# Kernel optimization log

Measured on AMD Instinct MI355X. Metric: run time of the kernel, lower is better.

## Reference

```python
import jax, jax.numpy as jnp
import numpy as np
import math

BN, NA, NE = 8192, 15, 16
DO, DA, DE = 96, 88, 80
H, NH = 512, 8
A_MOVE = 6


def _mha(q_in, kv, mask, Wq, Wk, Wv, Wo, n_heads):
    # q_in: [B,H] single query; kv: [B,L,H]; mask: [B,L] bool (True = valid)
    B, Hd = q_in.shape
    Hh = Hd // n_heads
    q = (q_in @ Wq).reshape(B, n_heads, 1, Hh)
    k = (kv @ Wk).reshape(B, -1, n_heads, Hh).transpose(0, 2, 1, 3)  # [B,nh,L,Hh]
    v = (kv @ Wv).reshape(B, -1, n_heads, Hh).transpose(0, 2, 1, 3)
    scores = jnp.einsum('bhqd,bhkd->bhqk', q, k) / math.sqrt(Hh)
    scores = jnp.where(mask[:, None, None, :], scores, -1e9)
    attn = jax.nn.softmax(scores, axis=-1)
    out = jnp.einsum('bhqk,bhkd->bhqd', attn, v).reshape(B, Hd)
    return out @ Wo


def _gru_cell(x, h, W_ih, W_hh, b_ih, b_hh):
    # torch GRU cell math. x: [B,3H], h: [B,H]
    gi = x @ W_ih.T + b_ih  # [B,3H]
    gh = h @ W_hh.T + b_hh  # [B,3H]
    i_r, i_z, i_n = jnp.split(gi, 3, axis=-1)
    h_r, h_z, h_n = jnp.split(gh, 3, axis=-1)
    r = jax.nn.sigmoid(i_r + h_r)
    z = jax.nn.sigmoid(i_z + h_z)
    n = jnp.tanh(i_n + r * h_n)
    return (1.0 - z) * n + z * h


def setup_inputs() -> dict:
    key = jax.random.key(0)
    ks = jax.random.split(key, 24)
    s = 0.02
    inp = {
        'own': jax.random.normal(ks[0], (BN, 1, DO), jnp.float32),
        'ally': jax.random.normal(ks[1], (BN, NA, DA), jnp.float32),
        'enemy': jax.random.normal(ks[2], (BN, NE, DE), jnp.float32),
        'prev_h': jax.random.normal(ks[3], (BN, H), jnp.float32),
        'W_own': jax.random.normal(ks[4], (DO, H), jnp.float32) * s,
        'b_own': jnp.zeros((H,), jnp.float32),
        'W_ally': jax.random.normal(ks[5], (DA, H), jnp.float32) * s,
        'b_ally': jnp.zeros((H,), jnp.float32),
        'W_enemy': jax.random.normal(ks[6], (DE, H), jnp.float32) * s,
        'b_enemy': jnp.zeros((H,), jnp.float32),
        'Wq_a': jax.random.normal(ks[7], (H, H), jnp.float32) * s,
        'Wk_a': jax.random.normal(ks[8], (H, H), jnp.float32) * s,
        'Wv_a': jax.random.normal(ks[9], (H, H), jnp.float32) * s,
        'Wo_a': jax.random.normal(ks[10], (H, H), jnp.float32) * s,
        'Wq_e': jax.random.normal(ks[11], (H, H), jnp.float32) * s,
        'Wk_e': jax.random.normal(ks[12], (H, H), jnp.float32) * s,
        'Wv_e': jax.random.normal(ks[13], (H, H), jnp.float32) * s,
        'Wo_e': jax.random.normal(ks[14], (H, H), jnp.float32) * s,
        'W_ih': jax.random.normal(ks[15], (3 * H, 3 * H), jnp.float32) * s,
        'W_hh': jax.random.normal(ks[16], (3 * H, H), jnp.float32) * s,
        'b_ih': jnp.zeros((3 * H,), jnp.float32),
        'b_hh': jnp.zeros((3 * H,), jnp.float32),
        'W_q': jax.random.normal(ks[17], (H, A_MOVE + NE), jnp.float32) * s,
        'b_q': jnp.zeros((A_MOVE + NE,), jnp.float32),
    }
    return inp


def reference(own, ally, enemy, prev_h,
              W_own, b_own, W_ally, b_ally, W_enemy, b_enemy,
              Wq_a, Wk_a, Wv_a, Wo_a, Wq_e, Wk_e, Wv_e, Wo_e,
              W_ih, W_hh, b_ih, b_hh, W_q, b_q):
    # masks: entity valid iff not all-zero feature row
    ally_mask = ~jnp.all(ally == 0, axis=-1)    # [B,NA]
    enemy_mask = ~jnp.all(enemy == 0, axis=-1)  # [B,NE]

    e_own = (own @ W_own + b_own)[:, 0, :]      # [B,H]
    A = ally @ W_ally + b_ally                   # [B,NA,H]
    E = enemy @ W_enemy + b_enemy                # [B,NE,H]

    zA = _mha(e_own, A, ally_mask, Wq_a, Wk_a, Wv_a, Wo_a, NH)
    zE = _mha(e_own, E, enemy_mask, Wq_e, Wk_e, Wv_e, Wo_e, NH)

    x = jnp.concatenate([e_own, zA, zE], axis=-1)  # [B,3H]
    h = _gru_cell(x, prev_h, W_ih, W_hh, b_ih, b_hh)
    q = h @ W_q + b_q                              # [B, A_move + NE]
    return q
```

## Files before the change

kernel.cpp:

```cpp
#include <hip/hip_runtime.h>
#include <cstdint>


typedef unsigned short bf16_t;
typedef __attribute__((ext_vector_type(8))) short bf16x8;
typedef __attribute__((ext_vector_type(4))) float f32x4;

__device__ inline float bf2f(bf16_t v) { return __uint_as_float(((unsigned)v) << 16); }
__device__ inline bf16_t f2bf(float x) {
    unsigned u = __float_as_uint(x);
    u += 0x7fffu + ((u >> 16) & 1u);
    return (bf16_t)(u >> 16);
}
__device__ inline void gload16(const bf16_t* g, bf16_t* l) {
    __builtin_amdgcn_global_load_lds(
        (const __attribute__((address_space(1))) void*)g,
        (__attribute__((address_space(3))) void*)l, 16, 0, 0);
}
__device__ inline int imin(int a, int b) { return a < b ? a : b; }

struct CJob { const float* s; bf16_t* d; int n4; };
template <int NJ> struct CJobs { CJob j[NJ]; };

template <int NJ>
__global__ __launch_bounds__(256)
void cvt_plain(CJobs<NJ> T)
{
    CJob jb = T.j[blockIdx.y];
    int stride = gridDim.x * 256;
    for (int i = blockIdx.x * 256 + threadIdx.x; i < jb.n4; i += stride) {
        float4 v = ((const float4*)jb.s)[i];
        ushort4 u; u.x = f2bf(v.x); u.y = f2bf(v.y); u.z = f2bf(v.z); u.w = f2bf(v.w);
        ((ushort4*)jb.d)[i] = u;
    }
}

struct TJob { const float* s; bf16_t* d; int R, C; };
template <int NJ> struct TJobs { TJob j[NJ]; };

template <int NJ>
__global__ __launch_bounds__(256)
void cvt_trans(TJobs<NJ> T)
{
    TJob jb = T.j[blockIdx.z];
    int c0 = blockIdx.x * 32, r0 = blockIdx.y * 32;
    if (c0 >= jb.C || r0 >= jb.R) return;
    __shared__ float t[32][33];
    int tx = threadIdx.x & 31, ty = threadIdx.x >> 5;
    for (int i = ty; i < 32; i += 8) {
        int r = r0 + i, c = c0 + tx;
        t[i][tx] = (r < jb.R && c < jb.C) ? jb.s[(int64_t)r * jb.C + c] : 0.f;
    }
    __syncthreads();
    for (int i = ty; i < 32; i += 8) {
        int c = c0 + i, r = r0 + tx;
        if (c < jb.C && r < jb.R) jb.d[(int64_t)c * jb.R + r] = f2bf(t[tx][i]);
    }
}

struct MJob { const bf16_t* A; const bf16_t* Bm; const float* bias; bf16_t* C;
              int lda, ldb, ldc, M, N, K, c32; };
template <int NJ> struct MJobs { MJob j[NJ]; };

template <int NJ>
__global__ __launch_bounds__(256)
void mfma_multi(MJobs<NJ> T)
{
    const MJob jb = T.j[blockIdx.z];
    const int m0 = blockIdx.x * 64, n0 = blockIdx.y * 64;
    if (m0 >= jb.M || n0 >= jb.N) return;
    __shared__ bf16_t As[64][32];
    __shared__ bf16_t Bs[64][32];
    const int tid = threadIdx.x;
    const int wv = tid >> 6, lane = tid & 63;
    const int fr = lane & 15, fq = lane >> 4;
    const int wm = (wv & 1) * 32, wn = (wv >> 1) * 32;
    const int lrow = tid >> 2;
    const int sw = ((lrow >> 1) & 3) ^ (tid & 3);
    const int ar = imin(m0 + lrow, jb.M - 1);
    const int br = imin(n0 + lrow, jb.N - 1);
    const bf16_t* gA = jb.A + (int64_t)ar * jb.lda + sw * 8;
    const bf16_t* gB = jb.Bm + (int64_t)br * jb.ldb + sw * 8;
    bf16_t* lA = &As[wv * 16][0];
    bf16_t* lB = &Bs[wv * 16][0];
    f32x4 acc[2][2] = {};
    for (int k0 = 0; k0 < jb.K; k0 += 32) {
        gload16(gA, lA);
        gload16(gB, lB);
        gA += 32; gB += 32;
        __syncthreads();
        bf16x8 aF[2], bF[2];
#pragma unroll
        for (int i = 0; i < 2; ++i) {
            int rw = wm + i * 16 + fr;
            aF[i] = *(const bf16x8*)&As[rw][(fq ^ ((rw >> 1) & 3)) * 8];
            int rn = wn + i * 16 + fr;
            bF[i] = *(const bf16x8*)&Bs[rn][(fq ^ ((rn >> 1) & 3)) * 8];
        }
#pragma unroll
        for (int i = 0; i < 2; ++i)
#pragma unroll
            for (int j = 0; j < 2; ++j)
                acc[i][j] = __builtin_amdgcn_mfma_f32_16x16x32_bf16(aF[i], bF[j], acc[i][j], 0, 0, 0);
        __syncthreads();
    }
#pragma unroll
    for (int j = 0; j < 2; ++j) {
        const int col = n0 + wn + j * 16 + fr;
        if (col >= jb.N) continue;
        const float bv = jb.bias ? jb.bias[col] : 0.f;
#pragma unroll
        for (int i = 0; i < 2; ++i) {
            const int rowb = m0 + wm + i * 16 + fq * 4;
#pragma unroll
            for (int r = 0; r < 4; ++r) {
                const int row = rowb + r;
                if (row >= jb.M) continue;
                const float v = acc[i][j][r] + bv;
                if (jb.c32) ((float*)jb.C)[(int64_t)row * jb.ldc + col] = v;
                else jb.C[(int64_t)row * jb.ldc + col] = f2bf(v);
            }
        }
    }
}

__global__ __launch_bounds__(256)
void mfma_nt(const bf16_t* __restrict__ A, int lda,
             const bf16_t* __restrict__ Bm, int ldb,
             bf16_t* __restrict__ C, int ldc,
             const float* __restrict__ bias, int K)
{
    __shared__ bf16_t As[128][32];
    __shared__ bf16_t Bs[128][32];
    const int tid = threadIdx.x;
    const int wv = tid >> 6, lane = tid & 63;
    const int fr = lane & 15, fq = lane >> 4;
    const int m0 = blockIdx.x * 128, n0 = blockIdx.y * 128;
    const int wm = (wv & 1) * 64, wn = (wv >> 1) * 64;
    const int lrow = tid >> 2;
    const int sw = ((lrow >> 1) & 3) ^ (tid & 3);
    f32x4 acc[4][4] = {};
    const bf16_t* gA = A + (int64_t)(m0 + lrow) * lda + sw * 8;
    const bf16_t* gB = Bm + (int64_t)(n0 + lrow) * ldb + sw * 8;
    bf16_t* lA0 = &As[wv * 16][0];
    bf16_t* lA1 = &As[64 + wv * 16][0];
    bf16_t* lB0 = &Bs[wv * 16][0];
    bf16_t* lB1 = &Bs[64 + wv * 16][0];
    const int64_t a64 = (int64_t)64 * lda, b64 = (int64_t)64 * ldb;
    for (int k0 = 0; k0 < K; k0 += 32) {
        gload16(gA, lA0);
        gload16(gA + a64, lA1);
        gload16(gB, lB0);
        gload16(gB + b64, lB1);
        gA += 32; gB += 32;
        __syncthreads();
        bf16x8 aF[4], bF[4];
#pragma unroll
        for (int i = 0; i < 4; ++i) {
            int rw = wm + i * 16 + fr;
            aF[i] = *(const bf16x8*)&As[rw][(fq ^ ((rw >> 1) & 3)) * 8];
            int rn = wn + i * 16 + fr;
            bF[i] = *(const bf16x8*)&Bs[rn][(fq ^ ((rn >> 1) & 3)) * 8];
        }
#pragma unroll
        for (int i = 0; i < 4; ++i)
#pragma unroll
            for (int j = 0; j < 4; ++j)
                acc[i][j] = __builtin_amdgcn_mfma_f32_16x16x32_bf16(aF[i], bF[j], acc[i][j], 0, 0, 0);
        __syncthreads();
    }
#pragma unroll
    for (int j = 0; j < 4; ++j) {
        const int col = n0 + wn + j * 16 + fr;
        const float bv = bias[col];
#pragma unroll
        for (int i = 0; i < 4; ++i) {
            const int row = m0 + wm + i * 16 + fq * 4;
#pragma unroll
            for (int r = 0; r < 4; ++r)
                C[(int64_t)(row + r) * ldc + col] = f2bf(acc[i][j][r] + bv);
        }
    }
}

__global__ __launch_bounds__(256)
void bias_fuse(const float* __restrict__ b_own, const float* __restrict__ b_ally,
               const float* __restrict__ b_enemy,
               const float* __restrict__ Wq_a, const float* __restrict__ Wq_e,
               const float* __restrict__ Wk_a, const float* __restrict__ Wv_a,
               const float* __restrict__ Wk_e, const float* __restrict__ Wv_e,
               float* __restrict__ fb)
{
    int job = blockIdx.x;
    int n = blockIdx.y * 64 + (threadIdx.x >> 2), q = threadIdx.x & 3;
    const float* v; const float* W;
    switch (job) {
        case 0: v = b_own;   W = Wq_a; break;
        case 1: v = b_own;   W = Wq_e; break;
        case 2: v = b_ally;  W = Wk_a; break;
        case 3: v = b_ally;  W = Wv_a; break;
        case 4: v = b_enemy; W = Wk_e; break;
        default: v = b_enemy; W = Wv_e; break;
    }
    float s = 0.f;
    for (int h = q * 128; h < q * 128 + 128; ++h)
        s = fmaf(v[h], W[(int64_t)h * 512 + n], s);
    s += __shfl_xor(s, 1);
    s += __shfl_xor(s, 2);
    if (q == 0) fb[job * 512 + n] = s;
}

__global__ __launch_bounds__(256)
void fixups(const float* __restrict__ fb, bf16_t* __restrict__ FkAB, bf16_t* __restrict__ FkEB,
            float* __restrict__ b2ab, const float* __restrict__ b_ih,
            const float* __restrict__ b_own, const float* __restrict__ W_ih,
            const bf16_t* __restrict__ WfaB, const bf16_t* __restrict__ WfeB,
            float* __restrict__ biasgi)
{
    int blk = blockIdx.x, t = threadIdx.x;
    if (blk < 2) {
        int i = blk * 256 + t;
        FkAB[88 * 512 + i] = f2bf(fb[2 * 512 + i]);
        FkEB[80 * 512 + i] = f2bf(fb[4 * 512 + i]);
    } else if (blk < 8) {
        int idx = (blk - 2) * 256 + t;
        if (idx < 1472) {
            int side = idx / 736, rem = idx - side * 736;
            int z = rem / 92, c = rem - z * 92;
            const bf16_t* Fk = side ? FkEB : FkAB;
            const float* bq = fb + side * 512;
            const float* bk = fb + (side ? 4 : 2) * 512;
            int BROW = side ? 80 : 88;
            float s = 0.f;
            for (int d = 0; d < 64; ++d) {
                float kv = (c == BROW) ? bk[z * 64 + d] : bf2f(Fk[c * 512 + z * 64 + d]);
                s = fmaf(bq[z * 64 + d], kv, s);
            }
            b2ab[(side * 8 + z) * 92 + c] = s;
        }
    } else {
        int j = (blk - 8) * 64 + (t >> 2), q = t & 3;
        float s = 0.f;
        for (int k = q * 128; k < q * 128 + 128; ++k) {
            s = fmaf(b_own[k],        W_ih[(int64_t)j * 1536 + k], s);
            s = fmaf(fb[3 * 512 + k], bf2f(WfaB[j * 512 + k]), s);
            s = fmaf(fb[5 * 512 + k], bf2f(WfeB[j * 512 + k]), s);
        }
        s += __shfl_xor(s, 1);
        s += __shfl_xor(s, 2);
        if (q == 0) biasgi[j] = s + b_ih[j];
    }
}

template <int NENT, int DF, int OFF, bool COPYOWN>
__global__ __launch_bounds__(128)
void attn_mid(const float* __restrict__ ent, const bf16_t* __restrict__ Kq,
              const bf16_t* __restrict__ ownB, bf16_t* __restrict__ acat, int B)
{
    const int b = blockIdx.x, tid = threadIdx.x;
    __shared__ float sent[NENT * DF];
    __shared__ float sKq[8 * (DF + 1)];
    __shared__ float ssc[8][NENT];
    __shared__ int smask[NENT];

    const float* eb = ent + (int64_t)b * NENT * DF;
    for (int i = tid; i < NENT * DF; i += 128) sent[i] = eb[i];
    for (int i = tid; i < 8 * (DF + 1); i += 128) {
        int h = i / (DF + 1), c = i - h * (DF + 1);
        sKq[i] = bf2f(Kq[((int64_t)h * B + b) * 92 + c]);
    }
    __syncthreads();
    if (tid < NENT) {
        int any = 0;
        for (int c = 0; c < DF; ++c) any |= (sent[tid * DF + c] != 0.f);
        smask[tid] = any;
    }
    __syncthreads();
    for (int t = tid; t < 8 * NENT; t += 128) {
        int h = t / NENT, i = t - h * NENT;
        const float* kqh = &sKq[h * (DF + 1)];
        float s = 0.f;
        for (int c = 0; c < DF; ++c) s = fmaf(sent[i * DF + c], kqh[c], s);
        s = (s + kqh[DF]) * 0.125f;
        if (!smask[i]) s = -1e9f;
        ssc[h][i] = s;
    }
    __syncthreads();
    if (tid < 8) {
        float m = -INFINITY;
        for (int i = 0; i < NENT; ++i) m = fmaxf(m, ssc[tid][i]);
        float e[NENT], sum = 0.f;
        for (int i = 0; i < NENT; ++i) { e[i] = expf(ssc[tid][i] - m); sum += e[i]; }
        float inv = 1.f / sum;
        for (int i = 0; i < NENT; ++i) ssc[tid][i] = e[i] * inv;
    }
    __syncthreads();
    bf16_t* arow = acat + (int64_t)b * 1440;
    if (COPYOWN) {
        for (int c = tid; c < 96; c += 128) arow[c] = ownB[(int64_t)b * 96 + c];
    }
    for (int t = tid; t < 8 * DF; t += 128) {
        int h = t / DF, c = t - h * DF;
        float s = 0.f;
        for (int i = 0; i < NENT; ++i) s = fmaf(ssc[h][i], sent[i * DF + c], s);
        arow[OFF + h * DF + c] = f2bf(s);
    }
}

__global__ __launch_bounds__(256)
void gru_final(const bf16_t* __restrict__ gi, const bf16_t* __restrict__ gh,
               const float* __restrict__ ph, const bf16_t* __restrict__ Wq,
               const float* __restrict__ bq, float* __restrict__ out, int B)
{
    const int b = blockIdx.x, tid = threadIdx.x;
    __shared__ float sh[512];
    const bf16_t* gib = gi + (int64_t)b * 1536;
    const bf16_t* ghb = gh + (int64_t)b * 1536;
    const float* phb = ph + (int64_t)b * 512;
    for (int n = tid; n < 512; n += 256) {
        float r = 1.f / (1.f + expf(-(bf2f(gib[n]) + bf2f(ghb[n]))));
        float z = 1.f / (1.f + expf(-(bf2f(gib[512 + n]) + bf2f(ghb[512 + n]))));
        float nn = tanhf(bf2f(gib[1024 + n]) + r * bf2f(ghb[1024 + n]));
        sh[n] = (1.f - z) * nn + z * phb[n];
    }
    __syncthreads();
    if (tid < 176) {
        int j = tid >> 3, l = tid & 7;
        float s = 0.f;
        for (int k = l; k < 512; k += 8) s = fmaf(sh[k], bf2f(Wq[j * 512 + k]), s);
        s += __shfl_down(s, 4, 64);
        s += __shfl_down(s, 2, 64);
        s += __shfl_down(s, 1, 64);
        if (l == 0) out[(int64_t)b * 22 + j] = s + bq[j];
    }
}

extern "C" void kernel_launch(void* const* d_in, const int* in_sizes, int n_in,
                              void* d_out, int out_size, void* d_ws, size_t ws_size,
                              hipStream_t stream)
{
    const float* own    = (const float*)d_in[0];
    const float* ally   = (const float*)d_in[1];
    const float* enemy  = (const float*)d_in[2];
    const float* prev_h = (const float*)d_in[3];
    const float* W_own  = (const float*)d_in[4];
    const float* b_own  = (const float*)d_in[5];
    const float* W_ally = (const float*)d_in[6];
    const float* b_ally = (const float*)d_in[7];
    const float* W_enemy= (const float*)d_in[8];
    const float* b_enemy= (const float*)d_in[9];
    const float* Wq_a   = (const float*)d_in[10];
    const float* Wk_a   = (const float*)d_in[11];
    const float* Wv_a   = (const float*)d_in[12];
    const float* Wo_a   = (const float*)d_in[13];
    const float* Wq_e   = (const float*)d_in[14];
    const float* Wk_e   = (const float*)d_in[15];
    const float* Wv_e   = (const float*)d_in[16];
    const float* Wo_e   = (const float*)d_in[17];
    const float* W_ih   = (const float*)d_in[18];
    const float* W_hh   = (const float*)d_in[19];
    const float* b_ih   = (const float*)d_in[20];
    const float* b_hh   = (const float*)d_in[21];
    const float* W_q    = (const float*)d_in[22];
    const float* b_q    = (const float*)d_in[23];
    float* outq = (float*)d_out;
    (void)n_in; (void)out_size;

    const int B = in_sizes[0] / 96;

    float* w = (float*)d_ws;
    size_t o = 0;
    auto alloc = [&](size_t n) { float* p = w + o; o += (n + 3) & ~(size_t)3; return p; };
    bf16_t* WqT[6];
    for (int i = 0; i < 6; ++i) WqT[i] = (bf16_t*)alloc(131072);
    bf16_t* WoaB  = (bf16_t*)alloc(131072);
    bf16_t* WoeB  = (bf16_t*)alloc(131072);
    bf16_t* WihB  = (bf16_t*)alloc(1179648);
    bf16_t* WhhB  = (bf16_t*)alloc(393216);
    bf16_t* WownB = (bf16_t*)alloc(24576);
    bf16_t* WallyB= (bf16_t*)alloc(22528);
    bf16_t* WenemyB=(bf16_t*)alloc(20480);
    bf16_t* ownB  = (bf16_t*)alloc(393216);
    bf16_t* FqaB  = (bf16_t*)alloc(24576);
    bf16_t* FqeB  = (bf16_t*)alloc(24576);
    bf16_t* FkAB  = (bf16_t*)alloc(23552);
    bf16_t* FkEB  = (bf16_t*)alloc(23552);
    bf16_t* FvAB  = (bf16_t*)alloc(22528);
    bf16_t* FvEB  = (bf16_t*)alloc(20480);
    bf16_t* WfaB  = (bf16_t*)alloc(393216);
    bf16_t* WfeB  = (bf16_t*)alloc(393216);
    bf16_t* MmB   = (bf16_t*)alloc(70656);
    float*  b2ab  = alloc(1472);
    float*  fb    = alloc(3072);
    bf16_t* Kq    = (bf16_t*)alloc((size_t)8 * B * 92 / 2);
    bf16_t* prevhB= (bf16_t*)w;
    bf16_t* gi    = (bf16_t*)w;
    if (o < (size_t)B * 1536 / 2) return;
    float*  biasgi= alloc(1536);
    bf16_t* WqTq  = (bf16_t*)alloc(5632);
    bf16_t* UTb   = (bf16_t*)alloc(1105920);
    bf16_t* A_cat = (bf16_t*)alloc((size_t)B * 1440 / 2);
    bf16_t* ghB   = (bf16_t*)alloc((size_t)B * 1536 / 2);

    if (ws_size < o * sizeof(float)) return;

    {
        CJobs<8> T;
        T.j[0] = { W_ih,    WihB,    589824 };
        T.j[1] = { W_hh,    WhhB,    196608 };
        T.j[2] = { Wo_a,    WoaB,     65536 };
        T.j[3] = { Wo_e,    WoeB,     65536 };
        T.j[4] = { W_own,   WownB,    12288 };
        T.j[5] = { W_ally,  WallyB,   11264 };
        T.j[6] = { W_enemy, WenemyB,  10240 };
        T.j[7] = { own,     ownB,    196608 };
        hipLaunchKernelGGL((cvt_plain<8>), dim3(128, 8), dim3(256), 0, stream, T);
    }
    {
        TJobs<7> T;
        T.j[0] = { Wq_a, WqT[0], 512, 512 };
        T.j[1] = { Wq_e, WqT[1], 512, 512 };
        T.j[2] = { Wk_a, WqT[2], 512, 512 };
        T.j[3] = { Wk_e, WqT[3], 512, 512 };
        T.j[4] = { Wv_a, WqT[4], 512, 512 };
        T.j[5] = { Wv_e, WqT[5], 512, 512 };
        T.j[6] = { W_q,  WqTq,   512,  22 };
        hipLaunchKernelGGL((cvt_trans<7>), dim3(16, 16, 7), dim3(256), 0, stream, T);
    }
    hipLaunchKernelGGL(bias_fuse, dim3(6, 8), dim3(256), 0, stream,
                       b_own, b_ally, b_enemy, Wq_a, Wq_e, Wk_a, Wv_a, Wk_e, Wv_e, fb);
    {
        MJobs<8> T;
        T.j[0] = { WownB,        WqT[0], nullptr, FqaB, 512, 512, 512,   96, 512, 512, 0 };
        T.j[1] = { WownB,        WqT[1], nullptr, FqeB, 512, 512, 512,   96, 512, 512, 0 };
        T.j[2] = { WallyB,       WqT[2], nullptr, FkAB, 512, 512, 512,   88, 512, 512, 0 };
        T.j[3] = { WenemyB,      WqT[3], nullptr, FkEB, 512, 512, 512,   80, 512, 512, 0 };
        T.j[4] = { WallyB,       WqT[4], nullptr, FvAB, 512, 512, 512,   88, 512, 512, 0 };
        T.j[5] = { WenemyB,      WqT[5], nullptr, FvEB, 512, 512, 512,   80, 512, 512, 0 };
        T.j[6] = { WihB + 512,   WoaB,   nullptr, WfaB, 1536, 512, 512, 1536, 512, 512, 0 };
        T.j[7] = { WihB + 1024,  WoeB,   nullptr, WfeB, 1536, 512, 512, 1536, 512, 512, 0 };
        hipLaunchKernelGGL((mfma_multi<8>), dim3(24, 8, 8), dim3(256), 0, stream, T);
    }
    hipLaunchKernelGGL(fixups, dim3(32), dim3(256), 0, stream,
                       fb, FkAB, FkEB, b2ab, b_ih, b_own, W_ih, WfaB, WfeB, biasgi);
    {
        MJobs<33> T;
        for (int h = 0; h < 8; ++h) {
            T.j[h]     = { FkAB + h * 64, FqaB + h * 64, nullptr, MmB + h * 92 * 96,
                           512, 512, 96, 92, 96, 64, 0 };
            T.j[8 + h] = { FkEB + h * 64, FqeB + h * 64, nullptr, MmB + (8 + h) * 92 * 96,
                           512, 512, 96, 92, 96, 64, 0 };
        }
        T.j[16] = { WihB, WownB, nullptr, UTb, 1536, 512, 1440, 1536, 96, 512, 0 };
        for (int h = 0; h < 8; ++h) {
            T.j[17 + h] = { WfaB + h * 64, FvAB + h * 64, nullptr, UTb + 96 + h * 88,
                            512, 512, 1440, 1536, 88, 64, 0 };
            T.j[25 + h] = { WfeB + h * 64, FvEB + h * 64, nullptr, UTb + 800 + h * 80,
                            512, 512, 1440, 1536, 80, 64, 0 };
        }
        hipLaunchKernelGGL((mfma_multi<33>), dim3(24, 2, 33), dim3(256), 0, stream, T);
    }
    {
        CJobs<1> T;
        T.j[0] = { prev_h, prevhB, B * 512 / 4 };
        hipLaunchKernelGGL((cvt_plain<1>), dim3(512, 1), dim3(256), 0, stream, T);
    }
    hipLaunchKernelGGL(mfma_nt, dim3(B / 128, 12), dim3(256), 0, stream,
                       prevhB, 512, WhhB, 512, ghB, 1536, b_hh, 512);
    {
        MJobs<8> T;
        for (int h = 0; h < 8; ++h)
            T.j[h] = { ownB, MmB + h * 92 * 96, b2ab + h * 92, Kq + (size_t)h * B * 92,
                       96, 96, 92, B, 92, 96, 0 };
        hipLaunchKernelGGL((mfma_multi<8>), dim3(B / 64, 2, 8), dim3(256), 0, stream, T);
    }
    hipLaunchKernelGGL((attn_mid<15, 88, 96, true>), dim3(B), dim3(128), 0, stream,
                       ally, Kq, ownB, A_cat, B);
    {
        MJobs<8> T;
        for (int h = 0; h < 8; ++h)
            T.j[h] = { ownB, MmB + (8 + h) * 92 * 96, b2ab + (8 + h) * 92, Kq + (size_t)h * B * 92,
                       96, 96, 92, B, 92, 96, 0 };
        hipLaunchKernelGGL((mfma_multi<8>), dim3(B / 64, 2, 8), dim3(256), 0, stream, T);
    }
    hipLaunchKernelGGL((attn_mid<16, 80, 800, false>), dim3(B), dim3(128), 0, stream,
                       enemy, Kq, ownB, A_cat, B);
    hipLaunchKernelGGL(mfma_nt, dim3(B / 128, 12), dim3(256), 0, stream,
                       A_cat, 1440, UTb, 1440, gi, 1536, biasgi, 1440);
    hipLaunchKernelGGL(gru_final, dim3(B), dim3(256), 0, stream,
                       gi, ghB, prev_h, WqTq, b_q, outq, B);
}
```

Before: 451.0 us.

## Replace scalar attention kernel with per-wave MFMA attention and batched Kq GEMM

The old attention stage ran one scalar kernel per batch row and built the per-head query-key projections with an 8-job multi GEMM. The new code does scores and the weighted value sum with bf16 MFMA, one wave per batch row and four rows per block, and computes Kq for all heads in a single mfma_nt GEMM into a padded 96-wide layout. The per-head bias vector is padded to match that layout. The goal is to remove the scalar FMA cost and the low occupancy of the old attention. In exchange, entity features are rounded to bf16 before attention, which may change accuracy slightly.

Result: faster. 403.1 us (-10.6%).

```diff
diff --git a/kernel.cpp b/kernel.cpp
--- a/kernel.cpp
+++ b/kernel.cpp
@@ -183,6 +183,106 @@
     }
 }
 
+template <int NENT, int DF, int OFF, bool COPYOWN>
+__global__ __launch_bounds__(256)
+void attn_mfma(const float* __restrict__ ent, const bf16_t* __restrict__ Kq,
+               const bf16_t* __restrict__ ownB, bf16_t* __restrict__ acat)
+{
+    __shared__ bf16_t sent[4][16][104];
+    __shared__ bf16_t sentT[4][96][24];
+    __shared__ bf16_t pbuf[4][16][24];
+    __shared__ float  maskf[4][16];
+
+    const int wv = threadIdx.x >> 6, lane = threadIdx.x & 63;
+    const int b = blockIdx.x * 4 + wv;
+    const int fr = lane & 15, g = lane >> 4;
+    const bf16x8 z8 = {0, 0, 0, 0, 0, 0, 0, 0};
+
+    if (lane < 16) maskf[wv][lane] = -1e9f;
+    const float* eb = ent + (int64_t)b * NENT * DF;
+#pragma unroll
+    for (int t = 0; t < 3; ++t) {
+        int idx = lane + t * 64;
+        int i = idx / 12, c0 = (idx % 12) * 8;
+        float v[8];
+        bool data = (i < NENT) && (c0 < DF);
+        if (data) {
+            float4 a = *(const float4*)(eb + (int64_t)i * DF + c0);
+            float4 c = *(const float4*)(eb + (int64_t)i * DF + c0 + 4);
+            v[0] = a.x; v[1] = a.y; v[2] = a.z; v[3] = a.w;
+            v[4] = c.x; v[5] = c.y; v[6] = c.z; v[7] = c.w;
+        } else {
+#pragma unroll
+            for (int j = 0; j < 8; ++j) v[j] = 0.f;
+        }
+        bf16x8 pk;
+        bool any = false;
+#pragma unroll
+        for (int j = 0; j < 8; ++j) { pk[j] = (short)f2bf(v[j]); any = any || (v[j] != 0.f); }
+        *(bf16x8*)&sent[wv][i][c0] = pk;
+#pragma unroll
+        for (int j = 0; j < 8; ++j) sentT[wv][c0 + j][i] = (bf16_t)pk[j];
+        if (any) maskf[wv][i] = 0.f;
+    }
+    __syncthreads();
+
+    const bf16_t* kqr = Kq + (size_t)b * 768 + fr * 96;
+    const float biash = (fr < 8) ? bf2f(kqr[DF]) : 0.f;
+    f32x4 S = {};
+#pragma unroll
+    for (int m = 0; m < 3; ++m) {
+        int kc = m * 32 + g * 8;
+        bf16x8 af = *(const bf16x8*)&sent[wv][fr][kc];
+        bf16x8 kf = (fr < 8) ? *(const bf16x8*)(kqr + kc) : z8;
+        S = __builtin_amdgcn_mfma_f32_16x16x32_bf16(af, kf, S, 0, 0, 0);
+    }
+    float4 mk = *(const float4*)&maskf[wv][g * 4];
+    float s0 = (S[0] + biash) * 0.125f + mk.x;
+    float s1 = (S[1] + biash) * 0.125f + mk.y;
+    float s2 = (S[2] + biash) * 0.125f + mk.z;
+    float s3 = (S[3] + biash) * 0.125f + mk.w;
+    float mx = fmaxf(fmaxf(s0, s1), fmaxf(s2, s3));
+    mx = fmaxf(mx, __shfl_xor(mx, 16, 64));
+    mx = fmaxf(mx, __shfl_xor(mx, 32, 64));
+    float e0 = __expf(s0 - mx), e1 = __expf(s1 - mx);
+    float e2 = __expf(s2 - mx), e3 = __expf(s3 - mx);
+    float sum = e0 + e1 + e2 + e3;
+    sum += __shfl_xor(sum, 16, 64);
+    sum += __shfl_xor(sum, 32, 64);
+    float inv = 1.f / sum;
+    ushort4 pu;
+    pu.x = f2bf(e0 * inv); pu.y = f2bf(e1 * inv);
+    pu.z = f2bf(e2 * inv); pu.w = f2bf(e3 * inv);
+    *(ushort4*)&pbuf[wv][fr][g * 4] = pu;
+    __syncthreads();
+
+    bf16x8 pa = (g < 2) ? *(const bf16x8*)&pbuf[wv][fr][g * 8] : z8;
+    f32x4 o[6] = {};
+#pragma unroll
+    for (int t = 0; t < 6; ++t) {
+        bf16x8 bfv = (g < 2) ? *(const bf16x8*)&sentT[wv][t * 16 + fr][g * 8] : z8;
+        o[t] = __builtin_amdgcn_mfma_f32_16x16x32_bf16(pa, bfv, o[t], 0, 0, 0);
+    }
+    bf16_t* ob = &sent[wv][0][0];
+    if (g < 2) {
+#pragma unroll
+        for (int t = 0; t < 6; ++t)
+#pragma unroll
+            for (int r = 0; r < 4; ++r)
+                ob[(g * 4 + r) * 96 + t * 16 + fr] = f2bf(o[t][r]);
+    }
+    __syncthreads();
+
+    bf16_t* arow = acat + (int64_t)b * 1440;
+    if (COPYOWN && lane < 12)
+        *(bf16x8*)(arow + lane * 8) = *(const bf16x8*)(ownB + (int64_t)b * 96 + lane * 8);
+    constexpr int CH = DF / 8;
+    if (lane < 8 * CH) {
+        int hh = lane / CH, j = lane % CH;
+        *(bf16x8*)(arow + OFF + hh * DF + j * 8) = *(const bf16x8*)&ob[hh * 96 + j * 8];
+    }
+}
+
 __global__ __launch_bounds__(256)
 void bias_fuse(const float* __restrict__ b_own, const float* __restrict__ b_ally,
                const float* __restrict__ b_enemy,
@@ -212,7 +312,7 @@
 
 __global__ __launch_bounds__(256)
 void fixups(const float* __restrict__ fb, bf16_t* __restrict__ FkAB, bf16_t* __restrict__ FkEB,
-            float* __restrict__ b2ab, const float* __restrict__ b_ih,
+            float* __restrict__ b2f, const float* __restrict__ b_ih,
             const float* __restrict__ b_own, const float* __restrict__ W_ih,
             const bf16_t* __restrict__ WfaB, const bf16_t* __restrict__ WfeB,
             float* __restrict__ biasgi)
@@ -224,20 +324,20 @@
         FkEB[80 * 512 + i] = f2bf(fb[4 * 512 + i]);
     } else if (blk < 8) {
         int idx = (blk - 2) * 256 + t;
-        if (idx < 1472) {
-            int side = idx / 736, rem = idx - side * 736;
-            int z = rem / 92, c = rem - z * 92;
+        int side = idx / 768, n = idx - side * 768;
+        int z = n / 96, c = n - z * 96;
+        float s = 0.f;
+        if (c < 92) {
             const bf16_t* Fk = side ? FkEB : FkAB;
             const float* bq = fb + side * 512;
             const float* bk = fb + (side ? 4 : 2) * 512;
             int BROW = side ? 80 : 88;
-            float s = 0.f;
             for (int d = 0; d < 64; ++d) {
                 float kv = (c == BROW) ? bk[z * 64 + d] : bf2f(Fk[c * 512 + z * 64 + d]);
                 s = fmaf(bq[z * 64 + d], kv, s);
             }
-            b2ab[(side * 8 + z) * 92 + c] = s;
-        }
+        }
+        b2f[idx] = s;
     } else {
         int j = (blk - 8) * 64 + (t >> 2), q = t & 3;
         float s = 0.f;
@@ -249,61 +349,6 @@
         s += __shfl_xor(s, 1);
         s += __shfl_xor(s, 2);
         if (q == 0) biasgi[j] = s + b_ih[j];
-    }
-}
-
-template <int NENT, int DF, int OFF, bool COPYOWN>
-__global__ __launch_bounds__(128)
-void attn_mid(const float* __restrict__ ent, const bf16_t* __restrict__ Kq,
-              const bf16_t* __restrict__ ownB, bf16_t* __restrict__ acat, int B)
-{
-    const int b = blockIdx.x, tid = threadIdx.x;
-    __shared__ float sent[NENT * DF];
-    __shared__ float sKq[8 * (DF + 1)];
-    __shared__ float ssc[8][NENT];
-    __shared__ int smask[NENT];
-
-    const float* eb = ent + (int64_t)b * NENT * DF;
-    for (int i = tid; i < NENT * DF; i += 128) sent[i] = eb[i];
-    for (int i = tid; i < 8 * (DF + 1); i += 128) {
-        int h = i / (DF + 1), c = i - h * (DF + 1);
-        sKq[i] = bf2f(Kq[((int64_t)h * B + b) * 92 + c]);
-    }
-    __syncthreads();
-    if (tid < NENT) {
-        int any = 0;
-        for (int c = 0; c < DF; ++c) any |= (sent[tid * DF + c] != 0.f);
-        smask[tid] = any;
-    }
-    __syncthreads();
-    for (int t = tid; t < 8 * NENT; t += 128) {
-        int h = t / NENT, i = t - h * NENT;
-        const float* kqh = &sKq[h * (DF + 1)];
-        float s = 0.f;
-        for (int c = 0; c < DF; ++c) s = fmaf(sent[i * DF + c], kqh[c], s);
-        s = (s + kqh[DF]) * 0.125f;
-        if (!smask[i]) s = -1e9f;
-        ssc[h][i] = s;
-    }
-    __syncthreads();
-    if (tid < 8) {
-        float m = -INFINITY;
-        for (int i = 0; i < NENT; ++i) m = fmaxf(m, ssc[tid][i]);
-        float e[NENT], sum = 0.f;
-        for (int i = 0; i < NENT; ++i) { e[i] = expf(ssc[tid][i] - m); sum += e[i]; }
-        float inv = 1.f / sum;
-        for (int i = 0; i < NENT; ++i) ssc[tid][i] = e[i] * inv;
-    }
-    __syncthreads();
-    bf16_t* arow = acat + (int64_t)b * 1440;
-    if (COPYOWN) {
-        for (int c = tid; c < 96; c += 128) arow[c] = ownB[(int64_t)b * 96 + c];
-    }
-    for (int t = tid; t < 8 * DF; t += 128) {
-        int h = t / DF, c = t - h * DF;
-        float s = 0.f;
-        for (int i = 0; i < NENT; ++i) s = fmaf(ssc[h][i], sent[i * DF + c], s);
-        arow[OFF + h * DF + c] = f2bf(s);
     }
 }
 
@@ -389,10 +434,11 @@
     bf16_t* FvEB  = (bf16_t*)alloc(20480);
     bf16_t* WfaB  = (bf16_t*)alloc(393216);
     bf16_t* WfeB  = (bf16_t*)alloc(393216);
-    bf16_t* MmB   = (bf16_t*)alloc(70656);
-    float*  b2ab  = alloc(1472);
+    bf16_t* MmPa  = (bf16_t*)alloc(36864);
+    bf16_t* MmPe  = (bf16_t*)alloc(36864);
+    float*  b2f   = alloc(1536);
     float*  fb    = alloc(3072);
-    bf16_t* Kq    = (bf16_t*)alloc((size_t)8 * B * 92 / 2);
+    bf16_t* Kq    = (bf16_t*)alloc((size_t)B * 768 / 2);
     bf16_t* prevhB= (bf16_t*)w;
     bf16_t* gi    = (bf16_t*)w;
     if (o < (size_t)B * 1536 / 2) return;
@@ -442,13 +488,13 @@
         hipLaunchKernelGGL((mfma_multi<8>), dim3(24, 8, 8), dim3(256), 0, stream, T);
     }
     hipLaunchKernelGGL(fixups, dim3(32), dim3(256), 0, stream,
-                       fb, FkAB, FkEB, b2ab, b_ih, b_own, W_ih, WfaB, WfeB, biasgi);
+                       fb, FkAB, FkEB, b2f, b_ih, b_own, W_ih, WfaB, WfeB, biasgi);
     {
         MJobs<33> T;
         for (int h = 0; h < 8; ++h) {
-            T.j[h]     = { FkAB + h * 64, FqaB + h * 64, nullptr, MmB + h * 92 * 96,
+            T.j[h]     = { FkAB + h * 64, FqaB + h * 64, nullptr, MmPa + h * 9216,
                            512, 512, 96, 92, 96, 64, 0 };
-            T.j[8 + h] = { FkEB + h * 64, FqeB + h * 64, nullptr, MmB + (8 + h) * 92 * 96,
+            T.j[8 + h] = { FkEB + h * 64, FqeB + h * 64, nullptr, MmPe + h * 9216,
                            512, 512, 96, 92, 96, 64, 0 };
         }
         T.j[16] = { WihB, WownB, nullptr, UTb, 1536, 512, 1440, 1536, 96, 512, 0 };
@@ -467,24 +513,14 @@
     }
     hipLaunchKernelGGL(mfma_nt, dim3(B / 128, 12), dim3(256), 0, stream,
                        prevhB, 512, WhhB, 512, ghB, 1536, b_hh, 512);
-    {
-        MJobs<8> T;
-        for (int h = 0; h < 8; ++h)
-            T.j[h] = { ownB, MmB + h * 92 * 96, b2ab + h * 92, Kq + (size_t)h * B * 92,
-                       96, 96, 92, B, 92, 96, 0 };
-        hipLaunchKernelGGL((mfma_multi<8>), dim3(B / 64, 2, 8), dim3(256), 0, stream, T);
-    }
-    hipLaunchKernelGGL((attn_mid<15, 88, 96, true>), dim3(B), dim3(128), 0, stream,
-                       ally, Kq, ownB, A_cat, B);
-    {
-        MJobs<8> T;
-        for (int h = 0; h < 8; ++h)
-            T.j[h] = { ownB, MmB + (8 + h) * 92 * 96, b2ab + (8 + h) * 92, Kq + (size_t)h * B * 92,
-                       96, 96, 92, B, 92, 96, 0 };
-        hipLaunchKernelGGL((mfma_multi<8>), dim3(B / 64, 2, 8), dim3(256), 0, stream, T);
-    }
-    hipLaunchKernelGGL((attn_mid<16, 80, 800, false>), dim3(B), dim3(128), 0, stream,
-                       enemy, Kq, ownB, A_cat, B);
+    hipLaunchKernelGGL(mfma_nt, dim3(B / 128, 6), dim3(256), 0, stream,
+                       ownB, 96, MmPa, 96, Kq, 768, b2f, 96);
+    hipLaunchKernelGGL((attn_mfma<15, 88, 96, true>), dim3(B / 4), dim3(256), 0, stream,
+                       ally, Kq, ownB, A_cat);
+    hipLaunchKernelGGL(mfma_nt, dim3(B / 128, 6), dim3(256), 0, stream,
+                       ownB, 96, MmPe, 96, Kq, 768, b2f + 768, 96);
+    hipLaunchKernelGGL((attn_mfma<16, 80, 800, false>), dim3(B / 4), dim3(256), 0, stream,
+                       enemy, Kq, ownB, A_cat);
     hipLaunchKernelGGL(mfma_nt, dim3(B / 128, 12), dim3(256), 0, stream,
                        A_cat, 1440, UTb, 1440, gi, 1536, biasgi, 1440);
     hipLaunchKernelGGL(gru_final, dim3(B), dim3(256), 0, stream,
```
